# Kernel tuning notes

Hardware: AMD Instinct MI355X
Metric: run time of the kernel (lower is better)

Reference implementation:

```python
import jax, jax.numpy as jnp
import numpy as np

N_NODES = 100000
N_EDGES = 1600000
D_FEAT = 512
HIDDEN = 64
N_CLASS = 16
DROP_P = 0.5


def setup_inputs() -> dict:
    key = jax.random.key(0)
    ks = jax.random.split(key, 6)
    x = jax.random.normal(ks[0], (N_NODES, D_FEAT), dtype=jnp.float32)
    edge_index = jax.random.randint(ks[1], (2, N_EDGES), 0, N_NODES, dtype=jnp.int32)
    e_w = jax.random.uniform(ks[2], (N_EDGES,), dtype=jnp.float32)
    # Glorot-ish init for the two GCN layer weights, zero bias (PyG default)
    W1 = jax.random.normal(ks[3], (D_FEAT, HIDDEN), dtype=jnp.float32) / np.sqrt(D_FEAT)
    b1 = jnp.zeros((HIDDEN,), dtype=jnp.float32)
    W2 = jax.random.normal(ks[4], (HIDDEN, N_CLASS), dtype=jnp.float32) / np.sqrt(HIDDEN)
    b2 = jnp.zeros((N_CLASS,), dtype=jnp.float32)
    return {"x": x, "edge_index": edge_index, "e_w": e_w,
            "W1": W1, "b1": b1, "W2": W2, "b2": b2}


def _gcn_conv(x, src, dst, w, W, b, num_nodes):
    """PyG GCNConv: linear transform, then symmetric-normalized scatter-add."""
    h = x @ W                                   # [N, out]
    deg = jax.ops.segment_sum(w, dst, num_segments=num_nodes)   # weighted in-degree
    dis = jnp.where(deg > 0, jax.lax.rsqrt(jnp.maximum(deg, 1e-12)), 0.0)
    norm = dis[src] * w * dis[dst]              # [E_total]
    msg = h[src] * norm[:, None]                # gather + scale  [E_total, out]
    out = jax.ops.segment_sum(msg, dst, num_segments=num_nodes)  # scatter-add
    return out + b


def reference(x, edge_index, e_w, W1, b1, W2, b2):
    n = x.shape[0]
    # add self-loops with weight 1 (GCNConv default)
    loops = jnp.arange(n, dtype=edge_index.dtype)
    src = jnp.concatenate([edge_index[0], loops])
    dst = jnp.concatenate([edge_index[1], loops])
    w = jnp.concatenate([e_w, jnp.ones((n,), dtype=e_w.dtype)])

    h = _gcn_conv(x, src, dst, w, W1, b1, n)
    h = jax.nn.relu(h)
    # F.dropout default p=0.5, training=True: deterministic fixed mask here
    keep = jax.random.bernoulli(jax.random.key(42), 1.0 - DROP_P, h.shape)
    h = jnp.where(keep, h / (1.0 - DROP_P), 0.0)

    x_out = _gcn_conv(h, src, dst, w, W2, b2, n)
    return jax.nn.log_softmax(x_out, axis=1), x_out
```

## Files before the change

### kernel.cpp

```cpp
#include <hip/hip_runtime.h>
#include <stdint.h>

#define N_NODES 100000
#define N_EDGES 1600000
#define D_FEAT  512
#define HIDDEN  64
#define N_CLASS 16
#define CAP     64
#define NBKT    196
#define BCAP    10240
#define EPB     4096
#define NWG1    ((N_EDGES + EPB - 1) / EPB)

typedef __bf16 bf16_t;
typedef bf16_t bf16x8 __attribute__((ext_vector_type(8)));
typedef float  f32x4  __attribute__((ext_vector_type(4)));

__device__ __forceinline__ unsigned rotl32(unsigned x, int d) {
    return (x << d) | (x >> (32 - d));
}
__device__ __forceinline__ void tf_round(unsigned& x0, unsigned& x1, int r) {
    x0 += x1; x1 = rotl32(x1, r); x1 ^= x0;
}
__device__ __forceinline__ uint2 threefry_0_42(unsigned c0, unsigned c1) {
    const unsigned ks0 = 0u, ks1 = 42u, ks2 = 0x1BD11BDAu ^ 0u ^ 42u;
    unsigned x0 = c0 + ks0, x1 = c1 + ks1;
    tf_round(x0,x1,13); tf_round(x0,x1,15); tf_round(x0,x1,26); tf_round(x0,x1,6);
    x0 += ks1; x1 += ks2 + 1u;
    tf_round(x0,x1,17); tf_round(x0,x1,29); tf_round(x0,x1,16); tf_round(x0,x1,24);
    x0 += ks2; x1 += ks0 + 2u;
    tf_round(x0,x1,13); tf_round(x0,x1,15); tf_round(x0,x1,26); tf_round(x0,x1,6);
    x0 += ks0; x1 += ks1 + 3u;
    tf_round(x0,x1,17); tf_round(x0,x1,29); tf_round(x0,x1,16); tf_round(x0,x1,24);
    x0 += ks1; x1 += ks2 + 4u;
    tf_round(x0,x1,13); tf_round(x0,x1,15); tf_round(x0,x1,26); tf_round(x0,x1,6);
    x0 += ks2; x1 += ks0 + 5u;
    return make_uint2(x0, x1);
}

__launch_bounds__(256)
__global__ void k_bin(const int* __restrict__ src, const int* __restrict__ dst,
                      const float* __restrict__ w,
                      int* __restrict__ bucket_cursor, int2* __restrict__ bkt) {
    __shared__ int hist[NBKT];
    __shared__ int binbase[NBKT];
    __shared__ int bincur[NBKT];
    int tid = threadIdx.x;
    int c4 = blockIdx.x * (EPB / 4);
    for (int t = tid; t < NBKT; t += 256) { hist[t] = 0; bincur[t] = 0; }
    __syncthreads();
    #pragma unroll
    for (int i = 0; i < EPB / 1024; ++i) {
        int e4 = c4 + tid + 256 * i;
        if (e4 * 4 < N_EDGES) {
            int4 d = ((const int4*)dst)[e4];
            atomicAdd(&hist[d.x >> 9], 1);
            atomicAdd(&hist[d.y >> 9], 1);
            atomicAdd(&hist[d.z >> 9], 1);
            atomicAdd(&hist[d.w >> 9], 1);
        }
    }
    __syncthreads();
    for (int t = tid; t < NBKT; t += 256)
        binbase[t] = hist[t] ? atomicAdd(&bucket_cursor[t], hist[t]) : 0;
    __syncthreads();
    #pragma unroll
    for (int i = 0; i < EPB / 1024; ++i) {
        int e4 = c4 + tid + 256 * i;
        if (e4 * 4 < N_EDGES) {
            int4 s  = ((const int4*)src)[e4];
            int4 d  = ((const int4*)dst)[e4];
            int4 wv = ((const int4*)w)[e4];
            int ss[4] = {s.x, s.y, s.z, s.w};
            int dd[4] = {d.x, d.y, d.z, d.w};
            int ww[4] = {wv.x, wv.y, wv.z, wv.w};
            #pragma unroll
            for (int q = 0; q < 4; ++q) {
                int b = dd[q] >> 9;
                int rank = atomicAdd(&bincur[b], 1);
                int pos = binbase[b] + rank;
                if (pos < BCAP)
                    bkt[(size_t)b * BCAP + pos] =
                        make_int2(ss[q] | ((dd[q] & 511) << 17), ww[q]);
            }
        }
    }
}

__launch_bounds__(256)
__global__ void k_build(const int* __restrict__ bucket_cursor, const int2* __restrict__ bkt,
                        int2* __restrict__ slots, int* __restrict__ cursor,
                        float* __restrict__ dis) {
    __shared__ int   cur[512];
    __shared__ float dg[512];
    int b = blockIdx.x, tid = threadIdx.x;
    cur[tid] = 0; cur[tid + 256] = 0;
    dg[tid] = 0.f; dg[tid + 256] = 0.f;
    __syncthreads();
    int cnt = bucket_cursor[b]; if (cnt > BCAP) cnt = BCAP;
    for (int e = tid; e < cnt; e += 256) {
        int2 p = bkt[(size_t)b * BCAP + e];
        int dl = ((unsigned)p.x) >> 17;
        int s  = p.x & 0x1FFFF;
        int rank = atomicAdd(&cur[dl], 1);
        if (rank < CAP)
            slots[((((size_t)b << 9) | dl) << 6) + rank] = make_int2(s, p.y);
        atomicAdd(&dg[dl], __int_as_float(p.y));
    }
    __syncthreads();
    #pragma unroll
    for (int t = 0; t < 2; ++t) {
        int loc = tid + 256 * t;
        int node = (b << 9) + loc;
        if (node < N_NODES) {
            cursor[node] = cur[loc];
            dis[node] = rsqrtf(dg[loc] + 1.0f);
        }
    }
}

__global__ void k_prepw(const float* __restrict__ W1, bf16_t* __restrict__ Wfg) {
    int e = blockIdx.x * 256 + threadIdx.x;
    int k = e >> 6, col = e & 63;
    int kstep = k >> 5, gg = (k >> 3) & 3, e8 = k & 7;
    int cf = col >> 4, lane = (col & 15) | (gg << 4);
    Wfg[(((kstep << 2) + cf) << 9) + (lane << 3) + e8] = (bf16_t)W1[e];
}

__launch_bounds__(256)
__global__ void k_gemm1(const float* __restrict__ x, const bf16_t* __restrict__ Wfg,
                        float* __restrict__ h1) {
    __shared__ bf16_t Wf[16384];
    int tid = threadIdx.x;
    int w = tid >> 6, l = tid & 63;
    int r = l & 15, g = l >> 4;
    int wrow = blockIdx.x * 128 + w * 32;
    f32x4 acc[2][4] = {};
    const float* xp0 = x + (size_t)(wrow + r) * D_FEAT + 8 * g;
    const float* xp1 = x + (size_t)(wrow + 16 + r) * D_FEAT + 8 * g;
    bool ok0 = (wrow + r) < N_NODES;
    bool ok1 = (wrow + 16 + r) < N_NODES;

    #pragma unroll
    for (int h = 0; h < 2; ++h) {
        if (h) __syncthreads();
        {
            const int4* sW = (const int4*)(Wfg + h * 16384);
            int4* dW = (int4*)Wf;
            #pragma unroll
            for (int t = 0; t < 8; ++t) dW[tid + 256 * t] = sW[tid + 256 * t];
        }
        __syncthreads();
        #pragma unroll
        for (int t2 = 0; t2 < 8; ++t2) {
            int t = h * 8 + t2;
            float4 p0 = make_float4(0.f,0.f,0.f,0.f), q0 = p0, p1 = p0, q1 = p0;
            if (ok0) {
                p0 = *(const float4*)(xp0 + t * 32);
                q0 = *(const float4*)(xp0 + t * 32 + 4);
            }
            if (ok1) {
                p1 = *(const float4*)(xp1 + t * 32);
                q1 = *(const float4*)(xp1 + t * 32 + 4);
            }
            bf16x8 a0, a1;
            a0[0]=(bf16_t)p0.x; a0[1]=(bf16_t)p0.y; a0[2]=(bf16_t)p0.z; a0[3]=(bf16_t)p0.w;
            a0[4]=(bf16_t)q0.x; a0[5]=(bf16_t)q0.y; a0[6]=(bf16_t)q0.z; a0[7]=(bf16_t)q0.w;
            a1[0]=(bf16_t)p1.x; a1[1]=(bf16_t)p1.y; a1[2]=(bf16_t)p1.z; a1[3]=(bf16_t)p1.w;
            a1[4]=(bf16_t)q1.x; a1[5]=(bf16_t)q1.y; a1[6]=(bf16_t)q1.z; a1[7]=(bf16_t)q1.w;
            #pragma unroll
            for (int cf = 0; cf < 4; ++cf) {
                bf16x8 b = *(const bf16x8*)&Wf[(((t2 << 2) + cf) << 9) + (l << 3)];
                acc[0][cf] = __builtin_amdgcn_mfma_f32_16x16x32_bf16(a0, b, acc[0][cf], 0, 0, 0);
                acc[1][cf] = __builtin_amdgcn_mfma_f32_16x16x32_bf16(a1, b, acc[1][cf], 0, 0, 0);
            }
        }
    }
    #pragma unroll
    for (int rf = 0; rf < 2; ++rf)
        #pragma unroll
        for (int cf = 0; cf < 4; ++cf)
            #pragma unroll
            for (int q = 0; q < 4; ++q) {
                int row = wrow + rf * 16 + 4 * g + q;
                int col = cf * 16 + r;
                if (row < N_NODES) h1[(size_t)row * HIDDEN + col] = acc[rf][cf][q];
            }
}

__launch_bounds__(256)
__global__ void k_agg1(const float* __restrict__ h1, const int2* __restrict__ slots,
                       const int* __restrict__ cursor, const float* __restrict__ dis,
                       const float* __restrict__ b1, const float* __restrict__ W2,
                       float* __restrict__ g) {
    __shared__ float W2s[HIDDEN * 17];
    __shared__ float h2s[4][HIDDEN];
    int tid = threadIdx.x;
    #pragma unroll
    for (int t = 0; t < 4; ++t) {
        int e = tid + 256 * t;
        W2s[(e >> 4) * 17 + (e & 15)] = W2[e];
    }
    int i = (blockIdx.x * blockDim.x + tid) >> 6;
    int f = tid & 63;
    int w = tid >> 6;
    float val = 0.f;
    if (i < N_NODES) {
        float di = dis[i];
        float acc = di * di * h1[(size_t)i * HIDDEN + f];
        int cnt = cursor[i]; cnt = cnt > CAP ? CAP : cnt;
        const int2* sl = &slots[(size_t)i << 6];
        int p = 0;
        for (; p + 4 <= cnt; p += 4) {
            int2 e0 = sl[p], e1 = sl[p+1], e2 = sl[p+2], e3 = sl[p+3];
            float n0 = dis[e0.x] * __int_as_float(e0.y) * di;
            float n1 = dis[e1.x] * __int_as_float(e1.y) * di;
            float n2 = dis[e2.x] * __int_as_float(e2.y) * di;
            float n3 = dis[e3.x] * __int_as_float(e3.y) * di;
            float v0 = h1[(size_t)e0.x * HIDDEN + f];
            float v1 = h1[(size_t)e1.x * HIDDEN + f];
            float v2 = h1[(size_t)e2.x * HIDDEN + f];
            float v3 = h1[(size_t)e3.x * HIDDEN + f];
            acc += n0 * v0 + n1 * v1 + n2 * v2 + n3 * v3;
        }
        for (; p < cnt; ++p) {
            int2 e0 = sl[p];
            acc += dis[e0.x] * __int_as_float(e0.y) * di * h1[(size_t)e0.x * HIDDEN + f];
        }
        acc += b1[f];
        acc = fmaxf(acc, 0.f);
        unsigned idx = (unsigned)i * HIDDEN + f;
        uint2 rr = threefry_0_42(0u, idx);
        unsigned bits = rr.x ^ rr.y;
        val = (bits & 0x80000000u) ? 0.f : acc * 2.f;
    }
    h2s[w][f] = val;
    __syncthreads();
    int j = tid & 15, q = (tid >> 4) & 3;
    int node = blockIdx.x * 4 + w;
    float p = 0.f;
    #pragma unroll
    for (int ff = 0; ff < 16; ++ff) {
        int fr = q * 16 + ff;
        p += h2s[w][fr] * W2s[fr * 17 + j];
    }
    p += __shfl_xor(p, 16, 64);
    p += __shfl_xor(p, 32, 64);
    if (q == 0 && node < N_NODES) g[(size_t)node * N_CLASS + j] = p;
}

__launch_bounds__(256)
__global__ void k_out(const float* __restrict__ g, const int2* __restrict__ slots,
                      const int* __restrict__ cursor, const float* __restrict__ dis,
                      const float* __restrict__ b2, float* __restrict__ out) {
    int i = (blockIdx.x * blockDim.x + threadIdx.x) >> 4;
    int j = threadIdx.x & 15;
    if (i >= N_NODES) return;
    float di = dis[i];
    float acc = di * di * g[(size_t)i * N_CLASS + j];
    int cnt = cursor[i]; cnt = cnt > CAP ? CAP : cnt;
    const int2* sl = &slots[(size_t)i << 6];
    int p = 0;
    for (; p + 2 <= cnt; p += 2) {
        int2 e0 = sl[p], e1 = sl[p+1];
        float n0 = dis[e0.x] * __int_as_float(e0.y) * di;
        float n1 = dis[e1.x] * __int_as_float(e1.y) * di;
        acc += n0 * g[(size_t)e0.x * N_CLASS + j] + n1 * g[(size_t)e1.x * N_CLASS + j];
    }
    for (; p < cnt; ++p) {
        int2 e0 = sl[p];
        acc += dis[e0.x] * __int_as_float(e0.y) * di * g[(size_t)e0.x * N_CLASS + j];
    }
    acc += b2[j];
    float xo = acc;
    float m = acc;
    #pragma unroll
    for (int d = 1; d < 16; d <<= 1) m = fmaxf(m, __shfl_xor(m, d, 16));
    float ex = expf(acc - m);
    float s = ex;
    #pragma unroll
    for (int d = 1; d < 16; d <<= 1) s += __shfl_xor(s, d, 16);
    float ls = (acc - m) - logf(s);
    out[(size_t)i * N_CLASS + j] = ls;
    out[(size_t)N_NODES * N_CLASS + (size_t)i * N_CLASS + j] = xo;
}

extern "C" void kernel_launch(void* const* d_in, const int* in_sizes, int n_in,
                              void* d_out, int out_size, void* d_ws, size_t ws_size,
                              hipStream_t stream) {
    const float* x  = (const float*)d_in[0];
    const int*   ei = (const int*)d_in[1];
    const float* ew = (const float*)d_in[2];
    const float* W1 = (const float*)d_in[3];
    const float* b1 = (const float*)d_in[4];
    const float* W2 = (const float*)d_in[5];
    const float* b2 = (const float*)d_in[6];
    float* out = (float*)d_out;
    const int* src = ei;
    const int* dst = ei + N_EDGES;

    size_t off = 0;
    char* wsb = (char*)d_ws;
    auto alloc = [&](size_t n) -> char* {
        char* p = wsb + off;
        off = (off + n + 255) & ~(size_t)255;
        return p;
    };
    int*    cursor = (int*)   alloc((size_t)N_NODES * 4);
    float*  dis    = (float*) alloc((size_t)N_NODES * 4);
    int*    bcur   = (int*)   alloc(NBKT * 4);
    bf16_t* Wfg    = (bf16_t*)alloc(32768 * 2);
    int2*   slots  = (int2*)  alloc((size_t)N_NODES * CAP * 8);
    float*  h1     = (float*) alloc((size_t)N_NODES * HIDDEN * 4);
    int2*   bkt    = (int2*)  alloc((size_t)NBKT * BCAP * 8);
    float*  g      = (float*) alloc((size_t)N_NODES * N_CLASS * 4);

    hipMemsetAsync(bcur, 0, NBKT * 4, stream);

    k_prepw<<<128, 256, 0, stream>>>(W1, Wfg);
    k_bin  <<<NWG1, 256, 0, stream>>>(src, dst, ew, bcur, bkt);
    k_build<<<NBKT, 256, 0, stream>>>(bcur, bkt, slots, cursor, dis);
    k_gemm1<<<(N_NODES + 127) / 128, 256, 0, stream>>>(x, Wfg, h1);
    k_agg1 <<<(N_NODES + 3) / 4, 256, 0, stream>>>(h1, slots, cursor, dis, b1, W2, g);
    k_out  <<<(N_NODES * 16 + 255) / 256, 256, 0, stream>>>(g, slots, cursor, dis, b2, out);
}
```

Before: 223.7 us.

## Split neighbor lists across lane groups with float4 gathers in aggregation kernels

Both aggregation kernels now assign each node's neighbor list to four lane subgroups. Each subgroup strides through the edges and gathers a float4 of features, and the partial sums are combined with cross-lane shuffles. The self-loop term is folded into the edge loop as a virtual edge. This cuts the number of serial dependent gather iterations per wave and widens memory transactions. In exchange it adds shuffle reductions and divergent trip counts among the subgroups. k_out also computes the softmax on float4 chunks and writes vectorized outputs.

```diff
diff --git a/kernel.cpp b/kernel.cpp
--- a/kernel.cpp
+++ b/kernel.cpp
@@ -202,39 +202,41 @@
         W2s[(e >> 4) * 17 + (e & 15)] = W2[e];
     }
     int i = (blockIdx.x * blockDim.x + tid) >> 6;
-    int f = tid & 63;
+    int l = tid & 63;
     int w = tid >> 6;
-    float val = 0.f;
+    int grp = l >> 4, sub = l & 15, f4 = sub << 2;
     if (i < N_NODES) {
         float di = dis[i];
-        float acc = di * di * h1[(size_t)i * HIDDEN + f];
         int cnt = cursor[i]; cnt = cnt > CAP ? CAP : cnt;
         const int2* sl = &slots[(size_t)i << 6];
-        int p = 0;
-        for (; p + 4 <= cnt; p += 4) {
-            int2 e0 = sl[p], e1 = sl[p+1], e2 = sl[p+2], e3 = sl[p+3];
-            float n0 = dis[e0.x] * __int_as_float(e0.y) * di;
-            float n1 = dis[e1.x] * __int_as_float(e1.y) * di;
-            float n2 = dis[e2.x] * __int_as_float(e2.y) * di;
-            float n3 = dis[e3.x] * __int_as_float(e3.y) * di;
-            float v0 = h1[(size_t)e0.x * HIDDEN + f];
-            float v1 = h1[(size_t)e1.x * HIDDEN + f];
-            float v2 = h1[(size_t)e2.x * HIDDEN + f];
-            float v3 = h1[(size_t)e3.x * HIDDEN + f];
-            acc += n0 * v0 + n1 * v1 + n2 * v2 + n3 * v3;
-        }
-        for (; p < cnt; ++p) {
-            int2 e0 = sl[p];
-            acc += dis[e0.x] * __int_as_float(e0.y) * di * h1[(size_t)e0.x * HIDDEN + f];
-        }
-        acc += b1[f];
-        acc = fmaxf(acc, 0.f);
+        float4 acc = make_float4(0.f, 0.f, 0.f, 0.f);
+        for (int t = grp; t <= cnt; t += 4) {
+            int s; float norm;
+            if (t == 0) { s = i; norm = di * di; }
+            else {
+                int2 e0 = sl[t - 1];
+                s = e0.x;
+                norm = dis[s] * __int_as_float(e0.y) * di;
+            }
+            float4 v = *(const float4*)&h1[(size_t)s * HIDDEN + f4];
+            acc.x += norm * v.x; acc.y += norm * v.y;
+            acc.z += norm * v.z; acc.w += norm * v.w;
+        }
+        acc.x += __shfl_xor(acc.x, 16); acc.x += __shfl_xor(acc.x, 32);
+        acc.y += __shfl_xor(acc.y, 16); acc.y += __shfl_xor(acc.y, 32);
+        acc.z += __shfl_xor(acc.z, 16); acc.z += __shfl_xor(acc.z, 32);
+        acc.w += __shfl_xor(acc.w, 16); acc.w += __shfl_xor(acc.w, 32);
+        float av = (grp == 0) ? acc.x : (grp == 1) ? acc.y : (grp == 2) ? acc.z : acc.w;
+        int f = f4 + grp;
+        av += b1[f];
+        av = fmaxf(av, 0.f);
         unsigned idx = (unsigned)i * HIDDEN + f;
         uint2 rr = threefry_0_42(0u, idx);
         unsigned bits = rr.x ^ rr.y;
-        val = (bits & 0x80000000u) ? 0.f : acc * 2.f;
-    }
-    h2s[w][f] = val;
+        h2s[w][f] = (bits & 0x80000000u) ? 0.f : av * 2.f;
+    } else {
+        h2s[w][f4 + grp] = 0.f;
+    }
     __syncthreads();
     int j = tid & 15, q = (tid >> 4) & 3;
     int node = blockIdx.x * 4 + w;
@@ -253,36 +255,47 @@
 __global__ void k_out(const float* __restrict__ g, const int2* __restrict__ slots,
                       const int* __restrict__ cursor, const float* __restrict__ dis,
                       const float* __restrict__ b2, float* __restrict__ out) {
-    int i = (blockIdx.x * blockDim.x + threadIdx.x) >> 4;
-    int j = threadIdx.x & 15;
+    int tid = threadIdx.x;
+    int i = (blockIdx.x * blockDim.x + tid) >> 4;
     if (i >= N_NODES) return;
+    int ln = tid & 15;
+    int sub4 = ln >> 2, c4 = (ln & 3) << 2;
     float di = dis[i];
-    float acc = di * di * g[(size_t)i * N_CLASS + j];
     int cnt = cursor[i]; cnt = cnt > CAP ? CAP : cnt;
     const int2* sl = &slots[(size_t)i << 6];
-    int p = 0;
-    for (; p + 2 <= cnt; p += 2) {
-        int2 e0 = sl[p], e1 = sl[p+1];
-        float n0 = dis[e0.x] * __int_as_float(e0.y) * di;
-        float n1 = dis[e1.x] * __int_as_float(e1.y) * di;
-        acc += n0 * g[(size_t)e0.x * N_CLASS + j] + n1 * g[(size_t)e1.x * N_CLASS + j];
-    }
-    for (; p < cnt; ++p) {
-        int2 e0 = sl[p];
-        acc += dis[e0.x] * __int_as_float(e0.y) * di * g[(size_t)e0.x * N_CLASS + j];
-    }
-    acc += b2[j];
-    float xo = acc;
-    float m = acc;
-    #pragma unroll
-    for (int d = 1; d < 16; d <<= 1) m = fmaxf(m, __shfl_xor(m, d, 16));
-    float ex = expf(acc - m);
-    float s = ex;
-    #pragma unroll
-    for (int d = 1; d < 16; d <<= 1) s += __shfl_xor(s, d, 16);
-    float ls = (acc - m) - logf(s);
-    out[(size_t)i * N_CLASS + j] = ls;
-    out[(size_t)N_NODES * N_CLASS + (size_t)i * N_CLASS + j] = xo;
+    float4 acc = make_float4(0.f, 0.f, 0.f, 0.f);
+    for (int t = sub4; t <= cnt; t += 4) {
+        int s; float norm;
+        if (t == 0) { s = i; norm = di * di; }
+        else {
+            int2 e0 = sl[t - 1];
+            s = e0.x;
+            norm = dis[s] * __int_as_float(e0.y) * di;
+        }
+        float4 v = *(const float4*)&g[(size_t)s * N_CLASS + c4];
+        acc.x += norm * v.x; acc.y += norm * v.y;
+        acc.z += norm * v.z; acc.w += norm * v.w;
+    }
+    acc.x += __shfl_xor(acc.x, 4); acc.x += __shfl_xor(acc.x, 8);
+    acc.y += __shfl_xor(acc.y, 4); acc.y += __shfl_xor(acc.y, 8);
+    acc.z += __shfl_xor(acc.z, 4); acc.z += __shfl_xor(acc.z, 8);
+    acc.w += __shfl_xor(acc.w, 4); acc.w += __shfl_xor(acc.w, 8);
+    float4 bv = *(const float4*)&b2[c4];
+    float4 xo = make_float4(acc.x + bv.x, acc.y + bv.y, acc.z + bv.z, acc.w + bv.w);
+    float m = fmaxf(fmaxf(xo.x, xo.y), fmaxf(xo.z, xo.w));
+    m = fmaxf(m, __shfl_xor(m, 1));
+    m = fmaxf(m, __shfl_xor(m, 2));
+    float e0 = expf(xo.x - m), e1 = expf(xo.y - m);
+    float e2 = expf(xo.z - m), e3 = expf(xo.w - m);
+    float s = e0 + e1 + e2 + e3;
+    s += __shfl_xor(s, 1);
+    s += __shfl_xor(s, 2);
+    float lg = logf(s);
+    float4 ls = make_float4(xo.x - m - lg, xo.y - m - lg, xo.z - m - lg, xo.w - m - lg);
+    if (sub4 == 0) {
+        *(float4*)&out[(size_t)i * N_CLASS + c4] = ls;
+        *(float4*)&out[(size_t)N_NODES * N_CLASS + (size_t)i * N_CLASS + c4] = xo;
+    }
 }
 
 extern "C" void kernel_launch(void* const* d_in, const int* in_sizes, int n_in,
```

Result: slower. 234.0 us (+4.6%).

## Store hidden features in bf16 and read W1 fragments directly from global

Applied to the files above, without the earlier changes.

The first GEMM now writes its hidden activations as bf16 instead of fp32, which halves the write traffic and the random gather traffic in the first aggregation kernel. The GEMM also drops the shared-memory staging of the weight fragments and its barriers, loading B fragments straight from global memory (expected to stay cache-resident) inside a partially unrolled K loop. Rounding the hidden activations to bf16 adds some numerical error.

```diff
diff --git a/kernel.cpp b/kernel.cpp
--- a/kernel.cpp
+++ b/kernel.cpp
@@ -129,8 +129,7 @@
 
 __launch_bounds__(256)
 __global__ void k_gemm1(const float* __restrict__ x, const bf16_t* __restrict__ Wfg,
-                        float* __restrict__ h1) {
-    __shared__ bf16_t Wf[16384];
+                        bf16_t* __restrict__ h1) {
     int tid = threadIdx.x;
     int w = tid >> 6, l = tid & 63;
     int r = l & 15, g = l >> 4;
@@ -141,39 +140,27 @@
     bool ok0 = (wrow + r) < N_NODES;
     bool ok1 = (wrow + 16 + r) < N_NODES;
 
-    #pragma unroll
-    for (int h = 0; h < 2; ++h) {
-        if (h) __syncthreads();
-        {
-            const int4* sW = (const int4*)(Wfg + h * 16384);
-            int4* dW = (int4*)Wf;
-            #pragma unroll
-            for (int t = 0; t < 8; ++t) dW[tid + 256 * t] = sW[tid + 256 * t];
-        }
-        __syncthreads();
+    #pragma unroll 4
+    for (int t = 0; t < 16; ++t) {
+        float4 p0 = make_float4(0.f,0.f,0.f,0.f), q0 = p0, p1 = p0, q1 = p0;
+        if (ok0) {
+            p0 = *(const float4*)(xp0 + t * 32);
+            q0 = *(const float4*)(xp0 + t * 32 + 4);
+        }
+        if (ok1) {
+            p1 = *(const float4*)(xp1 + t * 32);
+            q1 = *(const float4*)(xp1 + t * 32 + 4);
+        }
+        bf16x8 a0, a1;
+        a0[0]=(bf16_t)p0.x; a0[1]=(bf16_t)p0.y; a0[2]=(bf16_t)p0.z; a0[3]=(bf16_t)p0.w;
+        a0[4]=(bf16_t)q0.x; a0[5]=(bf16_t)q0.y; a0[6]=(bf16_t)q0.z; a0[7]=(bf16_t)q0.w;
+        a1[0]=(bf16_t)p1.x; a1[1]=(bf16_t)p1.y; a1[2]=(bf16_t)p1.z; a1[3]=(bf16_t)p1.w;
+        a1[4]=(bf16_t)q1.x; a1[5]=(bf16_t)q1.y; a1[6]=(bf16_t)q1.z; a1[7]=(bf16_t)q1.w;
         #pragma unroll
-        for (int t2 = 0; t2 < 8; ++t2) {
-            int t = h * 8 + t2;
-            float4 p0 = make_float4(0.f,0.f,0.f,0.f), q0 = p0, p1 = p0, q1 = p0;
-            if (ok0) {
-                p0 = *(const float4*)(xp0 + t * 32);
-                q0 = *(const float4*)(xp0 + t * 32 + 4);
-            }
-            if (ok1) {
-                p1 = *(const float4*)(xp1 + t * 32);
-                q1 = *(const float4*)(xp1 + t * 32 + 4);
-            }
-            bf16x8 a0, a1;
-            a0[0]=(bf16_t)p0.x; a0[1]=(bf16_t)p0.y; a0[2]=(bf16_t)p0.z; a0[3]=(bf16_t)p0.w;
-            a0[4]=(bf16_t)q0.x; a0[5]=(bf16_t)q0.y; a0[6]=(bf16_t)q0.z; a0[7]=(bf16_t)q0.w;
-            a1[0]=(bf16_t)p1.x; a1[1]=(bf16_t)p1.y; a1[2]=(bf16_t)p1.z; a1[3]=(bf16_t)p1.w;
-            a1[4]=(bf16_t)q1.x; a1[5]=(bf16_t)q1.y; a1[6]=(bf16_t)q1.z; a1[7]=(bf16_t)q1.w;
-            #pragma unroll
-            for (int cf = 0; cf < 4; ++cf) {
-                bf16x8 b = *(const bf16x8*)&Wf[(((t2 << 2) + cf) << 9) + (l << 3)];
-                acc[0][cf] = __builtin_amdgcn_mfma_f32_16x16x32_bf16(a0, b, acc[0][cf], 0, 0, 0);
-                acc[1][cf] = __builtin_amdgcn_mfma_f32_16x16x32_bf16(a1, b, acc[1][cf], 0, 0, 0);
-            }
+        for (int cf = 0; cf < 4; ++cf) {
+            bf16x8 b = *(const bf16x8*)&Wfg[(((t << 2) + cf) << 9) + (l << 3)];
+            acc[0][cf] = __builtin_amdgcn_mfma_f32_16x16x32_bf16(a0, b, acc[0][cf], 0, 0, 0);
+            acc[1][cf] = __builtin_amdgcn_mfma_f32_16x16x32_bf16(a1, b, acc[1][cf], 0, 0, 0);
         }
     }
     #pragma unroll
@@ -184,12 +171,12 @@
             for (int q = 0; q < 4; ++q) {
                 int row = wrow + rf * 16 + 4 * g + q;
                 int col = cf * 16 + r;
-                if (row < N_NODES) h1[(size_t)row * HIDDEN + col] = acc[rf][cf][q];
+                if (row < N_NODES) h1[(size_t)row * HIDDEN + col] = (bf16_t)acc[rf][cf][q];
             }
 }
 
 __launch_bounds__(256)
-__global__ void k_agg1(const float* __restrict__ h1, const int2* __restrict__ slots,
+__global__ void k_agg1(const bf16_t* __restrict__ h1, const int2* __restrict__ slots,
                        const int* __restrict__ cursor, const float* __restrict__ dis,
                        const float* __restrict__ b1, const float* __restrict__ W2,
                        float* __restrict__ g) {
@@ -207,7 +194,7 @@
     float val = 0.f;
     if (i < N_NODES) {
         float di = dis[i];
-        float acc = di * di * h1[(size_t)i * HIDDEN + f];
+        float acc = di * di * (float)h1[(size_t)i * HIDDEN + f];
         int cnt = cursor[i]; cnt = cnt > CAP ? CAP : cnt;
         const int2* sl = &slots[(size_t)i << 6];
         int p = 0;
@@ -217,15 +204,15 @@
             float n1 = dis[e1.x] * __int_as_float(e1.y) * di;
             float n2 = dis[e2.x] * __int_as_float(e2.y) * di;
             float n3 = dis[e3.x] * __int_as_float(e3.y) * di;
-            float v0 = h1[(size_t)e0.x * HIDDEN + f];
-            float v1 = h1[(size_t)e1.x * HIDDEN + f];
-            float v2 = h1[(size_t)e2.x * HIDDEN + f];
-            float v3 = h1[(size_t)e3.x * HIDDEN + f];
+            float v0 = (float)h1[(size_t)e0.x * HIDDEN + f];
+            float v1 = (float)h1[(size_t)e1.x * HIDDEN + f];
+            float v2 = (float)h1[(size_t)e2.x * HIDDEN + f];
+            float v3 = (float)h1[(size_t)e3.x * HIDDEN + f];
             acc += n0 * v0 + n1 * v1 + n2 * v2 + n3 * v3;
         }
         for (; p < cnt; ++p) {
             int2 e0 = sl[p];
-            acc += dis[e0.x] * __int_as_float(e0.y) * di * h1[(size_t)e0.x * HIDDEN + f];
+            acc += dis[e0.x] * __int_as_float(e0.y) * di * (float)h1[(size_t)e0.x * HIDDEN + f];
         }
         acc += b1[f];
         acc = fmaxf(acc, 0.f);
@@ -311,7 +298,7 @@
     int*    bcur   = (int*)   alloc(NBKT * 4);
     bf16_t* Wfg    = (bf16_t*)alloc(32768 * 2);
     int2*   slots  = (int2*)  alloc((size_t)N_NODES * CAP * 8);
-    float*  h1     = (float*) alloc((size_t)N_NODES * HIDDEN * 4);
+    bf16_t* h1     = (bf16_t*)alloc((size_t)N_NODES * HIDDEN * 2);
     int2*   bkt    = (int2*)  alloc((size_t)NBKT * BCAP * 8);
     float*  g      = (float*) alloc((size_t)N_NODES * N_CLASS * 4);
 
```

Measured after the change: 221.6 us. About the same (-0.9%).

## Merge independent prep kernels, store h1 in bf16, split neighbor loop across half-waves

Applied to the files above, without the earlier changes.

Folds the W1 prep into the binning launch and runs the bucket build and the GEMM1 in one launch via block-index dispatch, removing two launch boundaries and letting independent work overlap. The hidden activations h1 are stored as bf16, halving the gather traffic in the aggregation. The aggregation now has each half-wave process alternate neighbors with packed bf16 pairs and combines them with a shuffle. The cost is reduced precision of h1 and a larger shared-memory footprint for the build blocks.

```diff
diff --git a/kernel.cpp b/kernel.cpp
--- a/kernel.cpp
+++ b/kernel.cpp
@@ -11,6 +11,7 @@
 #define BCAP    10240
 #define EPB     4096
 #define NWG1    ((N_EDGES + EPB - 1) / EPB)
+#define GEMM1_BLKS ((N_NODES + 127) / 128)
 
 typedef __bf16 bf16_t;
 typedef bf16_t bf16x8 __attribute__((ext_vector_type(8)));
@@ -39,14 +40,25 @@
 }
 
 __launch_bounds__(256)
-__global__ void k_bin(const int* __restrict__ src, const int* __restrict__ dst,
-                      const float* __restrict__ w,
-                      int* __restrict__ bucket_cursor, int2* __restrict__ bkt) {
+__global__ void k_prep_bin(const float* __restrict__ W1, bf16_t* __restrict__ Wfg,
+                           const int* __restrict__ src, const int* __restrict__ dst,
+                           const float* __restrict__ w,
+                           int* __restrict__ bucket_cursor, int2* __restrict__ bkt) {
     __shared__ int hist[NBKT];
     __shared__ int binbase[NBKT];
     __shared__ int bincur[NBKT];
     int tid = threadIdx.x;
-    int c4 = blockIdx.x * (EPB / 4);
+    int bid = blockIdx.x;
+    if (bid < 128) {
+        int e = bid * 256 + tid;
+        int k = e >> 6, col = e & 63;
+        int kstep = k >> 5, gg = (k >> 3) & 3, e8 = k & 7;
+        int cf = col >> 4, lane = (col & 15) | (gg << 4);
+        Wfg[(((kstep << 2) + cf) << 9) + (lane << 3) + e8] = (bf16_t)W1[e];
+        return;
+    }
+    int b0 = bid - 128;
+    int c4 = b0 * (EPB / 4);
     for (int t = tid; t < NBKT; t += 256) { hist[t] = 0; bincur[t] = 0; }
     __syncthreads();
     #pragma unroll
@@ -88,53 +100,50 @@
 }
 
 __launch_bounds__(256)
-__global__ void k_build(const int* __restrict__ bucket_cursor, const int2* __restrict__ bkt,
-                        int2* __restrict__ slots, int* __restrict__ cursor,
-                        float* __restrict__ dis) {
-    __shared__ int   cur[512];
-    __shared__ float dg[512];
-    int b = blockIdx.x, tid = threadIdx.x;
-    cur[tid] = 0; cur[tid + 256] = 0;
-    dg[tid] = 0.f; dg[tid + 256] = 0.f;
-    __syncthreads();
-    int cnt = bucket_cursor[b]; if (cnt > BCAP) cnt = BCAP;
-    for (int e = tid; e < cnt; e += 256) {
-        int2 p = bkt[(size_t)b * BCAP + e];
-        int dl = ((unsigned)p.x) >> 17;
-        int s  = p.x & 0x1FFFF;
-        int rank = atomicAdd(&cur[dl], 1);
-        if (rank < CAP)
-            slots[((((size_t)b << 9) | dl) << 6) + rank] = make_int2(s, p.y);
-        atomicAdd(&dg[dl], __int_as_float(p.y));
-    }
-    __syncthreads();
-    #pragma unroll
-    for (int t = 0; t < 2; ++t) {
-        int loc = tid + 256 * t;
-        int node = (b << 9) + loc;
-        if (node < N_NODES) {
-            cursor[node] = cur[loc];
-            dis[node] = rsqrtf(dg[loc] + 1.0f);
-        }
-    }
-}
-
-__global__ void k_prepw(const float* __restrict__ W1, bf16_t* __restrict__ Wfg) {
-    int e = blockIdx.x * 256 + threadIdx.x;
-    int k = e >> 6, col = e & 63;
-    int kstep = k >> 5, gg = (k >> 3) & 3, e8 = k & 7;
-    int cf = col >> 4, lane = (col & 15) | (gg << 4);
-    Wfg[(((kstep << 2) + cf) << 9) + (lane << 3) + e8] = (bf16_t)W1[e];
-}
-
-__launch_bounds__(256)
-__global__ void k_gemm1(const float* __restrict__ x, const bf16_t* __restrict__ Wfg,
-                        float* __restrict__ h1) {
-    __shared__ bf16_t Wf[16384];
+__global__ void k_build_gemm1(const int* __restrict__ bucket_cursor,
+                              const int2* __restrict__ bkt,
+                              int2* __restrict__ slots, int* __restrict__ cursor,
+                              float* __restrict__ dis,
+                              const float* __restrict__ x,
+                              const bf16_t* __restrict__ Wfg,
+                              bf16_t* __restrict__ h1) {
+    __shared__ __align__(16) char smem[32768];
     int tid = threadIdx.x;
+    int bid = blockIdx.x;
+    if (bid < NBKT) {
+        int* cur  = (int*)smem;
+        float* dg = (float*)(smem + 2048);
+        int b = bid;
+        cur[tid] = 0; cur[tid + 256] = 0;
+        dg[tid] = 0.f; dg[tid + 256] = 0.f;
+        __syncthreads();
+        int cnt = bucket_cursor[b]; if (cnt > BCAP) cnt = BCAP;
+        for (int e = tid; e < cnt; e += 256) {
+            int2 p = bkt[(size_t)b * BCAP + e];
+            int dl = ((unsigned)p.x) >> 17;
+            int s  = p.x & 0x1FFFF;
+            int rank = atomicAdd(&cur[dl], 1);
+            if (rank < CAP)
+                slots[((((size_t)b << 9) | dl) << 6) + rank] = make_int2(s, p.y);
+            atomicAdd(&dg[dl], __int_as_float(p.y));
+        }
+        __syncthreads();
+        #pragma unroll
+        for (int t = 0; t < 2; ++t) {
+            int loc = tid + 256 * t;
+            int node = (b << 9) + loc;
+            if (node < N_NODES) {
+                cursor[node] = cur[loc];
+                dis[node] = rsqrtf(dg[loc] + 1.0f);
+            }
+        }
+        return;
+    }
+    bf16_t* Wf = (bf16_t*)smem;
+    int gb = bid - NBKT;
     int w = tid >> 6, l = tid & 63;
     int r = l & 15, g = l >> 4;
-    int wrow = blockIdx.x * 128 + w * 32;
+    int wrow = gb * 128 + w * 32;
     f32x4 acc[2][4] = {};
     const float* xp0 = x + (size_t)(wrow + r) * D_FEAT + 8 * g;
     const float* xp1 = x + (size_t)(wrow + 16 + r) * D_FEAT + 8 * g;
@@ -184,12 +193,12 @@
             for (int q = 0; q < 4; ++q) {
                 int row = wrow + rf * 16 + 4 * g + q;
                 int col = cf * 16 + r;
-                if (row < N_NODES) h1[(size_t)row * HIDDEN + col] = acc[rf][cf][q];
+                if (row < N_NODES) h1[(size_t)row * HIDDEN + col] = (bf16_t)acc[rf][cf][q];
             }
 }
 
 __launch_bounds__(256)
-__global__ void k_agg1(const float* __restrict__ h1, const int2* __restrict__ slots,
+__global__ void k_agg1(const bf16_t* __restrict__ h1, const int2* __restrict__ slots,
                        const int* __restrict__ cursor, const float* __restrict__ dis,
                        const float* __restrict__ b1, const float* __restrict__ W2,
                        float* __restrict__ g) {
@@ -202,39 +211,40 @@
         W2s[(e >> 4) * 17 + (e & 15)] = W2[e];
     }
     int i = (blockIdx.x * blockDim.x + tid) >> 6;
-    int f = tid & 63;
+    int l = tid & 63;
     int w = tid >> 6;
-    float val = 0.f;
+    int h = l >> 5, s32 = l & 31;
     if (i < N_NODES) {
         float di = dis[i];
-        float acc = di * di * h1[(size_t)i * HIDDEN + f];
         int cnt = cursor[i]; cnt = cnt > CAP ? CAP : cnt;
         const int2* sl = &slots[(size_t)i << 6];
-        int p = 0;
-        for (; p + 4 <= cnt; p += 4) {
-            int2 e0 = sl[p], e1 = sl[p+1], e2 = sl[p+2], e3 = sl[p+3];
-            float n0 = dis[e0.x] * __int_as_float(e0.y) * di;
-            float n1 = dis[e1.x] * __int_as_float(e1.y) * di;
-            float n2 = dis[e2.x] * __int_as_float(e2.y) * di;
-            float n3 = dis[e3.x] * __int_as_float(e3.y) * di;
-            float v0 = h1[(size_t)e0.x * HIDDEN + f];
-            float v1 = h1[(size_t)e1.x * HIDDEN + f];
-            float v2 = h1[(size_t)e2.x * HIDDEN + f];
-            float v3 = h1[(size_t)e3.x * HIDDEN + f];
-            acc += n0 * v0 + n1 * v1 + n2 * v2 + n3 * v3;
-        }
-        for (; p < cnt; ++p) {
+        float a0 = 0.f, a1 = 0.f;
+        if (h == 0) {
+            unsigned v = *(const unsigned*)&h1[(size_t)i * HIDDEN + 2 * s32];
+            float n = di * di;
+            a0 = n * __uint_as_float(v << 16);
+            a1 = n * __uint_as_float(v & 0xffff0000u);
+        }
+        #pragma unroll 2
+        for (int p = h; p < cnt; p += 2) {
             int2 e0 = sl[p];
-            acc += dis[e0.x] * __int_as_float(e0.y) * di * h1[(size_t)e0.x * HIDDEN + f];
-        }
-        acc += b1[f];
-        acc = fmaxf(acc, 0.f);
+            float n = dis[e0.x] * __int_as_float(e0.y) * di;
+            unsigned v = *(const unsigned*)&h1[(size_t)e0.x * HIDDEN + 2 * s32];
+            a0 += n * __uint_as_float(v << 16);
+            a1 += n * __uint_as_float(v & 0xffff0000u);
+        }
+        a0 += __shfl_xor(a0, 32);
+        a1 += __shfl_xor(a1, 32);
+        int f = 2 * s32 + h;
+        float av = h ? a1 : a0;
+        av += b1[f];
+        av = fmaxf(av, 0.f);
         unsigned idx = (unsigned)i * HIDDEN + f;
         uint2 rr = threefry_0_42(0u, idx);
-        unsigned bits = rr.x ^ rr.y;
-        val = (bits & 0x80000000u) ? 0.f : acc * 2.f;
-    }
-    h2s[w][f] = val;
+        h2s[w][f] = ((rr.x ^ rr.y) & 0x80000000u) ? 0.f : av * 2.f;
+    } else {
+        h2s[w][2 * s32 + h] = 0.f;
+    }
     __syncthreads();
     int j = tid & 15, q = (tid >> 4) & 3;
     int node = blockIdx.x * 4 + w;
@@ -311,16 +321,15 @@
     int*    bcur   = (int*)   alloc(NBKT * 4);
     bf16_t* Wfg    = (bf16_t*)alloc(32768 * 2);
     int2*   slots  = (int2*)  alloc((size_t)N_NODES * CAP * 8);
-    float*  h1     = (float*) alloc((size_t)N_NODES * HIDDEN * 4);
+    bf16_t* h1     = (bf16_t*)alloc((size_t)N_NODES * HIDDEN * 2);
     int2*   bkt    = (int2*)  alloc((size_t)NBKT * BCAP * 8);
     float*  g      = (float*) alloc((size_t)N_NODES * N_CLASS * 4);
 
     hipMemsetAsync(bcur, 0, NBKT * 4, stream);
 
-    k_prepw<<<128, 256, 0, stream>>>(W1, Wfg);
-    k_bin  <<<NWG1, 256, 0, stream>>>(src, dst, ew, bcur, bkt);
-    k_build<<<NBKT, 256, 0, stream>>>(bcur, bkt, slots, cursor, dis);
-    k_gemm1<<<(N_NODES + 127) / 128, 256, 0, stream>>>(x, Wfg, h1);
-    k_agg1 <<<(N_NODES + 3) / 4, 256, 0, stream>>>(h1, slots, cursor, dis, b1, W2, g);
-    k_out  <<<(N_NODES * 16 + 255) / 256, 256, 0, stream>>>(g, slots, cursor, dis, b2, out);
-}
+    k_prep_bin   <<<128 + NWG1, 256, 0, stream>>>(W1, Wfg, src, dst, ew, bcur, bkt);
+    k_build_gemm1<<<NBKT + GEMM1_BLKS, 256, 0, stream>>>(bcur, bkt, slots, cursor, dis,
+                                                         x, Wfg, h1);
+    k_agg1<<<(N_NODES + 3) / 4, 256, 0, stream>>>(h1, slots, cursor, dis, b1, W2, g);
+    k_out <<<(N_NODES * 16 + 255) / 256, 256, 0, stream>>>(g, slots, cursor, dis, b2, out);
+}
```

New measurement: 203.3 us. 1.1x faster.
